# Performance work log

Measured on AMD Instinct MI355X. Metric: run time of the kernel, lower is better.

## Reference

```python
import jax, jax.numpy as jnp
import numpy as np

B, N = 256, 400
DIMENSIONS, VOCAB = 400, 2
T_DIM, H_DIM = 128, 256
EDGE_P = 0.05
LOG_MAX_POS = np.float32(np.log(10000.0))


def timestep_embedding(t, dim):
    # transformer sinusoidal embedding (DDPM/score-SDE style)
    half = dim // 2
    freqs = jnp.exp(-LOG_MAX_POS * jnp.arange(half, dtype=jnp.float32) / (half - 1))
    args = t[:, None] * freqs[None, :]  # [B, half]
    return jnp.concatenate([jnp.sin(args), jnp.cos(args)], axis=-1)  # [B, dim]


def gcn_norm_adj(adj):
    # PyG GCNConv: binary edges (dense_to_sparse values discarded), add self loops,
    # symmetric normalization. deg computed per target (column sums).
    A = (adj != 0).astype(adj.dtype)
    eye = jnp.eye(adj.shape[-1], dtype=adj.dtype)
    As = A + eye[None]                     # [B,N,N]
    deg = As.sum(axis=-2)                  # column sums, [B,N]; >=1 due to self loops
    dis = 1.0 / jnp.sqrt(deg)              # [B,N]
    # out[i] = dis[i] * sum_j As[j,i] * dis[j] * x[j]  ->  An = dis_i * As^T * dis_j
    return dis[:, :, None] * jnp.swapaxes(As, -1, -2) * dis[:, None, :]


def setup_inputs() -> dict:
    key = jax.random.key(0)
    k = jax.random.split(key, 8)
    # symmetric Bernoulli adjacency, no self loops
    up = jnp.triu(jax.random.bernoulli(k[0], EDGE_P, (B, N, N)), 1)
    adj = (up + jnp.swapaxes(up, -1, -2)).astype(jnp.float32)
    times = jax.random.uniform(k[1], (B,), dtype=jnp.float32)
    s = 0.05
    W1 = jax.random.normal(k[2], (T_DIM + 1, H_DIM), jnp.float32) * s
    b1 = jnp.zeros((H_DIM,), jnp.float32)
    W2 = jax.random.normal(k[3], (H_DIM, H_DIM), jnp.float32) * s
    b2 = jnp.zeros((H_DIM,), jnp.float32)
    Wlin = jax.random.normal(k[4], (H_DIM, DIMENSIONS * VOCAB), jnp.float32) * s
    blin = jnp.zeros((DIMENSIONS * VOCAB,), jnp.float32)
    return {"adj": adj, "times": times, "W1": W1, "b1": b1,
            "W2": W2, "b2": b2, "Wlin": Wlin, "blin": blin}


def reference(adj, times, W1, b1, W2, b2, Wlin, blin):
    b, n, _ = adj.shape
    node_degree = adj.sum(axis=1)[..., None]                     # [B,N,1]
    temb = timestep_embedding(times, T_DIM)                      # [B,T_DIM]
    temb = jnp.broadcast_to(temb[:, None, :], (b, n, T_DIM))     # [B,N,T_DIM]
    x = jnp.concatenate([node_degree, temb], axis=-1)            # [B,N,T_DIM+1]

    An = gcn_norm_adj(adj)                                       # [B,N,N]
    h = jnp.einsum('bij,bjh->bih', An, x @ W1) + b1              # GCNConv 1
    h = jax.nn.relu(h)
    h = jnp.einsum('bij,bjh->bih', An, h @ W2) + b2              # GCNConv 2
    h = jax.nn.relu(h)
    pooled = h.mean(axis=1)                                      # global mean pool [B,H]
    logits = pooled @ Wlin + blin                                # [B, D*V]
    return logits.reshape(b, DIMENSIONS, VOCAB)
```

## Files before the change

### kernel.cpp

```cpp
#include <hip/hip_runtime.h>
#include <cstdint>
#include <cstddef>

#define BATCH 256
#define NN 400
#define HH 256
#define TDIM 128
#define HALFD 64
#define OUTD 800
#define BITW 16
#define BMW 13
#define Y2S 424

using short8  = __attribute__((ext_vector_type(8))) short;
using short4v = __attribute__((ext_vector_type(4))) short;
using f32x4   = __attribute__((ext_vector_type(4))) float;

__device__ __forceinline__ short f2bf_trunc(float x) {
  union { float f; unsigned int u; } c; c.f = x; return (short)(c.u >> 16);
}
__device__ __forceinline__ short f2bf_rne(float x) {
  union { float f; unsigned int u; } c; c.f = x;
  unsigned int r = c.u + 0x7FFFu + ((c.u >> 16) & 1u);
  return (short)(r >> 16);
}

__global__ __launch_bounds__(256) void k_prep(const float* __restrict__ adj,
    unsigned int* __restrict__ bits, float* __restrict__ dis,
    float* __restrict__ dd) {
  int bg = blockIdx.x;
  int rbase = blockIdx.y * 16;
  int wv = threadIdx.x >> 6, lane = threadIdx.x & 63;
#pragma unroll
  for (int rr = 0; rr < 4; ++rr) {
    int i = rbase + wv * 4 + rr;
    const float* arow = adj + ((size_t)bg * NN + i) * NN;
    unsigned int b8 = 0; int c = 0;
    if (lane < 50) {
      float4 v0 = *(const float4*)(arow + 8 * lane);
      float4 v1 = *(const float4*)(arow + 8 * lane + 4);
      b8 = (v0.x != 0.f ? 1u : 0u) | (v0.y != 0.f ? 2u : 0u) |
           (v0.z != 0.f ? 4u : 0u) | (v0.w != 0.f ? 8u : 0u) |
           (v1.x != 0.f ? 16u : 0u) | (v1.y != 0.f ? 32u : 0u) |
           (v1.z != 0.f ? 64u : 0u) | (v1.w != 0.f ? 128u : 0u);
      c = __popc(b8);
      if ((i >> 3) == lane) b8 |= 1u << (i & 7);
    }
    int cs = c;
#pragma unroll
    for (int s = 32; s; s >>= 1) cs += __shfl_xor(cs, s);
    unsigned int p0 = (unsigned int)__shfl((int)b8, 4 * lane);
    unsigned int p1 = (unsigned int)__shfl((int)b8, 4 * lane + 1);
    unsigned int p2 = (unsigned int)__shfl((int)b8, 4 * lane + 2);
    unsigned int p3 = (unsigned int)__shfl((int)b8, 4 * lane + 3);
    if (lane < BITW)
      bits[((size_t)bg * NN + i) * BITW + lane] =
          (lane < BMW) ? (p0 | (p1 << 8) | (p2 << 16) | (p3 << 24)) : 0u;
    if (lane == 0) {
      float d = rsqrtf((float)cs + 1.f);
      dis[bg * NN + i] = d;
      dd[bg * NN + i] = d * (float)cs;
    }
  }
}

__global__ __launch_bounds__(256) void k_temb(
    const float* __restrict__ times, const float* __restrict__ W1,
    float* __restrict__ tproj) {
  int b = blockIdx.x, t = threadIdx.x;
  __shared__ float te[TDIM];
  if (t < HALFD) {
    float f = expf(-9.210340371976184f * (float)t / (float)(HALFD - 1));
    float arg = times[b] * f;
    te[t] = sinf(arg);
    te[t + HALFD] = cosf(arg);
  }
  __syncthreads();
  float acc = 0.f;
#pragma unroll 8
  for (int k = 0; k < TDIM; ++k) acc += te[k] * W1[(1 + k) * HH + t];
  tproj[b * HH + t] = acc;
}

__global__ __launch_bounds__(256) void k_w2s(const float* __restrict__ W2,
                                             short* __restrict__ W2s) {
  int t = threadIdx.x;
  int blk = blockIdx.x * 4 + (t >> 6);
  int lane = t & 63;
  int q = blk >> 5, k0 = (blk >> 2) & 7, f = blk & 3;
  int n = q * 64 + f * 16 + (lane & 15);
  int kb = k0 * 32 + (lane >> 4) * 8;
  short8 v;
#pragma unroll
  for (int e = 0; e < 8; ++e) v[e] = f2bf_rne(W2[(size_t)(kb + e) * HH + n]);
  *(short8*)(W2s + (size_t)blk * 512 + lane * 8) = v;
}

__global__ __launch_bounds__(512) void k_pq(const unsigned int* __restrict__ bits,
    const float* __restrict__ dis, const float* __restrict__ dd,
    float* __restrict__ pp, float* __restrict__ qq) {
  int bg = blockIdx.x, t = threadIdx.x;
  __shared__ float sd[NN], su[NN];
  for (int j = t; j < NN; j += 512) { sd[j] = dis[bg * NN + j]; su[j] = dd[bg * NN + j]; }
  __syncthreads();
  if (t >= NN) return;
  const uint4* bp = (const uint4*)(bits + ((size_t)bg * NN + t) * BITW);
  uint4 qa = bp[0], qb = bp[1], qc = bp[2];
  unsigned int wr[13] = {qa.x, qa.y, qa.z, qa.w, qb.x, qb.y, qb.z, qb.w,
                         qc.x, qc.y, qc.z, qc.w, ((const unsigned int*)bp)[12]};
  float ps = 0.f, qs = 0.f;
#pragma unroll
  for (int w = 0; w < BMW; ++w) {
    unsigned int u = wr[w];
    int base = w * 32;
    while (u) {
      int j = base + __builtin_ctz(u);
      u &= u - 1;
      ps += su[j]; qs += sd[j];
    }
  }
  float d = sd[t];
  pp[bg * NN + t] = d * ps;
  qq[bg * NN + t] = d * qs;
}

__global__ __launch_bounds__(512, 2) void k_fused(
    const unsigned int* __restrict__ bits, const float* __restrict__ disg,
    const float* __restrict__ ppg, const float* __restrict__ qqg,
    const short* __restrict__ W2s, const float* __restrict__ W1,
    const float* __restrict__ b1, const float* __restrict__ tproj,
    const float* __restrict__ b2, float* __restrict__ pooled) {
  extern __shared__ char smem[];
  short* y2q         = (short*)smem;
  unsigned int* bmpL = (unsigned int*)(smem + 54272);
  float* sd          = (float*)(smem + 75072);
  float* ppL         = (float*)(smem + 76672);
  float* qqL         = (float*)(smem + 78272);
  short* lut4        = (short*)(smem + 79872);
  float* pool        = (float*)(smem + 76672);

  int t = threadIdx.x;
  int wv = t >> 6, lane = t & 63, l15 = lane & 15, l4 = lane >> 4;
  int bg = blockIdx.x, q = blockIdx.y;

  if (t < NN) {
    const uint4* bp = (const uint4*)(bits + ((size_t)bg * NN + t) * BITW);
    uint4 qa = bp[0], qb = bp[1], qc = bp[2];
    bmpL[t * BMW + 0] = qa.x;  bmpL[t * BMW + 1] = qa.y;
    bmpL[t * BMW + 2] = qa.z;  bmpL[t * BMW + 3] = qa.w;
    bmpL[t * BMW + 4] = qb.x;  bmpL[t * BMW + 5] = qb.y;
    bmpL[t * BMW + 6] = qb.z;  bmpL[t * BMW + 7] = qb.w;
    bmpL[t * BMW + 8] = qc.x;  bmpL[t * BMW + 9] = qc.y;
    bmpL[t * BMW + 10] = qc.z; bmpL[t * BMW + 11] = qc.w;
    bmpL[t * BMW + 12] = ((const unsigned int*)bp)[12];
    sd[t] = disg[bg * NN + t];
    ppL[t] = ppg[bg * NN + t];
    qqL[t] = qqg[bg * NN + t];
  }
  if (t < 192) {
    int n = t / 3, c = t % 3;
    short8 z = {};
    *(short8*)(y2q + n * Y2S + 400 + c * 8) = z;
  }
  if (t < 16) {
    short4v v;
#pragma unroll
    for (int e = 0; e < 4; ++e) v[e] = ((t >> e) & 1) ? (short)0x3F80 : (short)0;
    *(short4v*)(lut4 + t * 4) = v;
  }
  __syncthreads();

  const float* tpr = tproj + bg * HH;
  const short* w2b = W2s + (size_t)q * 8 * 4 * 512;
  float pv[4], qv[4];
#pragma unroll
  for (int mi = 0; mi < 4; ++mi) {
    int mt = wv + mi * 8;
    int arow = mt * 16 + l15;
    pv[mi] = (mt < 25) ? ppL[arow] : 0.f;
    qv[mi] = (mt < 25) ? qqL[arow] : 0.f;
  }
  f32x4 acc[4][4];
#pragma unroll
  for (int mi = 0; mi < 4; ++mi)
#pragma unroll
    for (int f = 0; f < 4; ++f) acc[mi][f] = (f32x4){0.f, 0.f, 0.f, 0.f};

#pragma unroll
  for (int k0 = 0; k0 < 8; ++k0) {
    int kk = k0 * 32 + l4 * 8;
    float4 w1a = *(const float4*)(W1 + kk), w1b = *(const float4*)(W1 + kk + 4);
    float4 b1a = *(const float4*)(b1 + kk), b1b = *(const float4*)(b1 + kk + 4);
    float4 tpa = *(const float4*)(tpr + kk), tpb = *(const float4*)(tpr + kk + 4);
    short8 bf[4];
#pragma unroll
    for (int f = 0; f < 4; ++f)
      bf[f] = *(const short8*)(w2b + (size_t)(k0 * 4 + f) * 512 + lane * 8);
#pragma unroll
    for (int mi = 0; mi < 4; ++mi) {
      if (wv + mi * 8 < 25) {
        float ppv = pv[mi], qqv = qv[mi];
        short8 af;
        af[0] = f2bf_trunc(fmaxf(ppv * w1a.x + qqv * tpa.x + b1a.x, 0.f));
        af[1] = f2bf_trunc(fmaxf(ppv * w1a.y + qqv * tpa.y + b1a.y, 0.f));
        af[2] = f2bf_trunc(fmaxf(ppv * w1a.z + qqv * tpa.z + b1a.z, 0.f));
        af[3] = f2bf_trunc(fmaxf(ppv * w1a.w + qqv * tpa.w + b1a.w, 0.f));
        af[4] = f2bf_trunc(fmaxf(ppv * w1b.x + qqv * tpb.x + b1b.x, 0.f));
        af[5] = f2bf_trunc(fmaxf(ppv * w1b.y + qqv * tpb.y + b1b.y, 0.f));
        af[6] = f2bf_trunc(fmaxf(ppv * w1b.z + qqv * tpb.z + b1b.z, 0.f));
        af[7] = f2bf_trunc(fmaxf(ppv * w1b.w + qqv * tpb.w + b1b.w, 0.f));
#pragma unroll
        for (int f = 0; f < 4; ++f)
          acc[mi][f] = __builtin_amdgcn_mfma_f32_16x16x32_bf16(af, bf[f], acc[mi][f], 0, 0, 0);
      }
    }
  }
#pragma unroll
  for (int mi = 0; mi < 4; ++mi) {
    int mt = wv + mi * 8;
    if (mt < 25) {
      float4 d4 = *(const float4*)(sd + mt * 16 + l4 * 4);
#pragma unroll
      for (int f = 0; f < 4; ++f) {
        short4v pk;
        pk[0] = f2bf_trunc(d4.x * acc[mi][f][0]);
        pk[1] = f2bf_trunc(d4.y * acc[mi][f][1]);
        pk[2] = f2bf_trunc(d4.z * acc[mi][f][2]);
        pk[3] = f2bf_trunc(d4.w * acc[mi][f][3]);
        *(short4v*)(y2q + (f * 16 + l15) * Y2S + mt * 16 + l4 * 4) = pk;
      }
    }
  }
  __syncthreads();

  f32x4 acc2[4][4];
#pragma unroll
  for (int mi = 0; mi < 4; ++mi)
#pragma unroll
    for (int f = 0; f < 4; ++f) acc2[mi][f] = (f32x4){0.f, 0.f, 0.f, 0.f};

#pragma unroll
  for (int ks = 0; ks < 13; ++ks) {
    short8 bfv[4];
#pragma unroll
    for (int f = 0; f < 4; ++f)
      bfv[f] = *(const short8*)(y2q + (f * 16 + l15) * Y2S + ks * 32 + l4 * 8);
#pragma unroll
    for (int mi = 0; mi < 4; ++mi) {
      int mt = wv + mi * 8;
      if (mt < 25) {
        unsigned int wd = bmpL[(mt * 16 + l15) * BMW + ks];
        unsigned int byt = (wd >> (l4 * 8)) & 0xFFu;
        short4v lo = *(const short4v*)(lut4 + (byt & 15u) * 4);
        short4v hi = *(const short4v*)(lut4 + (byt >> 4) * 4);
        short8 af;
        af[0] = lo[0]; af[1] = lo[1]; af[2] = lo[2]; af[3] = lo[3];
        af[4] = hi[0]; af[5] = hi[1]; af[6] = hi[2]; af[7] = hi[3];
#pragma unroll
        for (int f = 0; f < 4; ++f)
          acc2[mi][f] = __builtin_amdgcn_mfma_f32_16x16x32_bf16(af, bfv[f], acc2[mi][f], 0, 0, 0);
      }
    }
  }

#pragma unroll
  for (int f = 0; f < 4; ++f) {
    float b2v = b2[q * 64 + f * 16 + l15];
    float s = 0.f;
#pragma unroll
    for (int mi = 0; mi < 4; ++mi) {
      int mt = wv + mi * 8;
      if (mt < 25) {
        float4 d4 = *(const float4*)(sd + mt * 16 + l4 * 4);
        s += fmaxf(d4.x * acc2[mi][f][0] + b2v, 0.f)
           + fmaxf(d4.y * acc2[mi][f][1] + b2v, 0.f)
           + fmaxf(d4.z * acc2[mi][f][2] + b2v, 0.f)
           + fmaxf(d4.w * acc2[mi][f][3] + b2v, 0.f);
      }
    }
    s += __shfl_xor(s, 16);
    s += __shfl_xor(s, 32);
    if (l4 == 0) pool[wv * 64 + f * 16 + l15] = s;
  }
  __syncthreads();
  if (t < 64) {
    float sum = 0.f;
#pragma unroll
    for (int w8 = 0; w8 < 8; ++w8) sum += pool[w8 * 64 + t];
    pooled[(size_t)bg * HH + q * 64 + t] = sum;
  }
}

__global__ __launch_bounds__(256) void k_out(
    const float* __restrict__ pooled, const float* __restrict__ Wlin,
    const float* __restrict__ blin, float* __restrict__ out) {
  int bb = blockIdx.x * 2, t = threadIdx.x;
  __shared__ float ps[2][HH];
  ps[0][t] = pooled[(size_t)bb * HH + t] * (1.f / 400.f);
  ps[1][t] = pooled[(size_t)(bb + 1) * HH + t] * (1.f / 400.f);
  __syncthreads();
#pragma unroll
  for (int c = 0; c < 4; ++c) {
    int o = t + c * 256;
    if (o < OUTD) {
      float a0 = blin[o], a1 = a0;
#pragma unroll 8
      for (int h = 0; h < HH; ++h) {
        float wv = Wlin[h * OUTD + o];
        a0 += ps[0][h] * wv;
        a1 += ps[1][h] * wv;
      }
      out[(size_t)bb * OUTD + o] = a0;
      out[(size_t)(bb + 1) * OUTD + o] = a1;
    }
  }
}

extern "C" void kernel_launch(void* const* d_in, const int* in_sizes, int n_in,
                              void* d_out, int out_size, void* d_ws, size_t ws_size,
                              hipStream_t stream) {
  const float* adj   = (const float*)d_in[0];
  const float* times = (const float*)d_in[1];
  const float* W1    = (const float*)d_in[2];
  const float* b1    = (const float*)d_in[3];
  const float* W2    = (const float*)d_in[4];
  const float* b2    = (const float*)d_in[5];
  const float* Wlin  = (const float*)d_in[6];
  const float* blin  = (const float*)d_in[7];
  float* out = (float*)d_out;

  char* ws = (char*)d_ws;
  size_t off = 0;
  auto alloc = [&](size_t bytes) -> void* {
    void* ptr = ws + off;
    off = (off + bytes + 255) & ~(size_t)255;
    return ptr;
  };
  float* dis    = (float*)alloc((size_t)BATCH * NN * 4);
  float* dd     = (float*)alloc((size_t)BATCH * NN * 4);
  float* pp     = (float*)alloc((size_t)BATCH * NN * 4);
  float* qq     = (float*)alloc((size_t)BATCH * NN * 4);
  float* tproj  = (float*)alloc((size_t)BATCH * HH * 4);
  float* pooled = (float*)alloc((size_t)BATCH * HH * 4);
  short* W2s    = (short*)alloc((size_t)128 * 512 * 2);
  unsigned int* bits = (unsigned int*)alloc((size_t)BATCH * NN * BITW * 4);

  k_temb<<<BATCH, 256, 0, stream>>>(times, W1, tproj);
  k_w2s<<<32, 256, 0, stream>>>(W2, W2s);
  k_prep<<<dim3(BATCH, 25), 256, 0, stream>>>(adj, bits, dis, dd);
  k_pq<<<BATCH, 512, 0, stream>>>(bits, dis, dd, pp, qq);
  k_fused<<<dim3(BATCH, 4), 512, 80000, stream>>>(
      bits, dis, pp, qq, W2s, W1, b1, tproj, b2, pooled);
  k_out<<<128, 256, 0, stream>>>(pooled, Wlin, blin, out);
}
```

Before: 150.3 us.

## Fold degree and pq computation into fused kernel, merge temb and W2 prep

Removes the separate k_pq kernel and the dis/dd/pp/qq global buffers. The fused kernel now computes degrees from the popcount of the bitmap rows (self loop included) and does the neighbour sums for p/q in shared memory. k_temb and k_w2s are merged into one launch, leaving four launches instead of six. In exchange, each of the 4 column-split blocks per graph redoes the pq computation, and shared memory grows to 81600 bytes.

```diff
diff --git a/kernel.cpp b/kernel.cpp
--- a/kernel.cpp
+++ b/kernel.cpp
@@ -26,8 +26,7 @@
 }
 
 __global__ __launch_bounds__(256) void k_prep(const float* __restrict__ adj,
-    unsigned int* __restrict__ bits, float* __restrict__ dis,
-    float* __restrict__ dd) {
+    unsigned int* __restrict__ bits) {
   int bg = blockIdx.x;
   int rbase = blockIdx.y * 16;
   int wv = threadIdx.x >> 6, lane = threadIdx.x & 63;
@@ -35,7 +34,7 @@
   for (int rr = 0; rr < 4; ++rr) {
     int i = rbase + wv * 4 + rr;
     const float* arow = adj + ((size_t)bg * NN + i) * NN;
-    unsigned int b8 = 0; int c = 0;
+    unsigned int b8 = 0;
     if (lane < 50) {
       float4 v0 = *(const float4*)(arow + 8 * lane);
       float4 v1 = *(const float4*)(arow + 8 * lane + 4);
@@ -43,100 +42,63 @@
            (v0.z != 0.f ? 4u : 0u) | (v0.w != 0.f ? 8u : 0u) |
            (v1.x != 0.f ? 16u : 0u) | (v1.y != 0.f ? 32u : 0u) |
            (v1.z != 0.f ? 64u : 0u) | (v1.w != 0.f ? 128u : 0u);
-      c = __popc(b8);
       if ((i >> 3) == lane) b8 |= 1u << (i & 7);
     }
-    int cs = c;
-#pragma unroll
-    for (int s = 32; s; s >>= 1) cs += __shfl_xor(cs, s);
     unsigned int p0 = (unsigned int)__shfl((int)b8, 4 * lane);
     unsigned int p1 = (unsigned int)__shfl((int)b8, 4 * lane + 1);
     unsigned int p2 = (unsigned int)__shfl((int)b8, 4 * lane + 2);
     unsigned int p3 = (unsigned int)__shfl((int)b8, 4 * lane + 3);
-    if (lane < BITW)
+    if (lane < BMW)
       bits[((size_t)bg * NN + i) * BITW + lane] =
-          (lane < BMW) ? (p0 | (p1 << 8) | (p2 << 16) | (p3 << 24)) : 0u;
-    if (lane == 0) {
-      float d = rsqrtf((float)cs + 1.f);
-      dis[bg * NN + i] = d;
-      dd[bg * NN + i] = d * (float)cs;
-    }
-  }
-}
-
-__global__ __launch_bounds__(256) void k_temb(
+          p0 | (p1 << 8) | (p2 << 16) | (p3 << 24);
+  }
+}
+
+__global__ __launch_bounds__(256) void k_tw(
     const float* __restrict__ times, const float* __restrict__ W1,
-    float* __restrict__ tproj) {
-  int b = blockIdx.x, t = threadIdx.x;
+    float* __restrict__ tproj, const float* __restrict__ W2,
+    short* __restrict__ W2s) {
   __shared__ float te[TDIM];
-  if (t < HALFD) {
-    float f = expf(-9.210340371976184f * (float)t / (float)(HALFD - 1));
-    float arg = times[b] * f;
-    te[t] = sinf(arg);
-    te[t + HALFD] = cosf(arg);
-  }
-  __syncthreads();
-  float acc = 0.f;
+  int t = threadIdx.x;
+  if (blockIdx.x < 256) {
+    int b = blockIdx.x;
+    if (t < HALFD) {
+      float f = expf(-9.210340371976184f * (float)t / (float)(HALFD - 1));
+      float arg = times[b] * f;
+      te[t] = sinf(arg);
+      te[t + HALFD] = cosf(arg);
+    }
+    __syncthreads();
+    float acc = 0.f;
 #pragma unroll 8
-  for (int k = 0; k < TDIM; ++k) acc += te[k] * W1[(1 + k) * HH + t];
-  tproj[b * HH + t] = acc;
-}
-
-__global__ __launch_bounds__(256) void k_w2s(const float* __restrict__ W2,
-                                             short* __restrict__ W2s) {
-  int t = threadIdx.x;
-  int blk = blockIdx.x * 4 + (t >> 6);
-  int lane = t & 63;
-  int q = blk >> 5, k0 = (blk >> 2) & 7, f = blk & 3;
-  int n = q * 64 + f * 16 + (lane & 15);
-  int kb = k0 * 32 + (lane >> 4) * 8;
-  short8 v;
-#pragma unroll
-  for (int e = 0; e < 8; ++e) v[e] = f2bf_rne(W2[(size_t)(kb + e) * HH + n]);
-  *(short8*)(W2s + (size_t)blk * 512 + lane * 8) = v;
-}
-
-__global__ __launch_bounds__(512) void k_pq(const unsigned int* __restrict__ bits,
-    const float* __restrict__ dis, const float* __restrict__ dd,
-    float* __restrict__ pp, float* __restrict__ qq) {
-  int bg = blockIdx.x, t = threadIdx.x;
-  __shared__ float sd[NN], su[NN];
-  for (int j = t; j < NN; j += 512) { sd[j] = dis[bg * NN + j]; su[j] = dd[bg * NN + j]; }
-  __syncthreads();
-  if (t >= NN) return;
-  const uint4* bp = (const uint4*)(bits + ((size_t)bg * NN + t) * BITW);
-  uint4 qa = bp[0], qb = bp[1], qc = bp[2];
-  unsigned int wr[13] = {qa.x, qa.y, qa.z, qa.w, qb.x, qb.y, qb.z, qb.w,
-                         qc.x, qc.y, qc.z, qc.w, ((const unsigned int*)bp)[12]};
-  float ps = 0.f, qs = 0.f;
-#pragma unroll
-  for (int w = 0; w < BMW; ++w) {
-    unsigned int u = wr[w];
-    int base = w * 32;
-    while (u) {
-      int j = base + __builtin_ctz(u);
-      u &= u - 1;
-      ps += su[j]; qs += sd[j];
-    }
-  }
-  float d = sd[t];
-  pp[bg * NN + t] = d * ps;
-  qq[bg * NN + t] = d * qs;
+    for (int k = 0; k < TDIM; ++k) acc += te[k] * W1[(1 + k) * HH + t];
+    tproj[b * HH + t] = acc;
+  } else {
+    int blk = (blockIdx.x - 256) * 4 + (t >> 6);
+    int lane = t & 63;
+    int q = blk >> 5, k0 = (blk >> 2) & 7, f = blk & 3;
+    int n = q * 64 + f * 16 + (lane & 15);
+    int kb = k0 * 32 + (lane >> 4) * 8;
+    short8 v;
+#pragma unroll
+    for (int e = 0; e < 8; ++e) v[e] = f2bf_rne(W2[(size_t)(kb + e) * HH + n]);
+    *(short8*)(W2s + (size_t)blk * 512 + lane * 8) = v;
+  }
 }
 
 __global__ __launch_bounds__(512, 2) void k_fused(
-    const unsigned int* __restrict__ bits, const float* __restrict__ disg,
-    const float* __restrict__ ppg, const float* __restrict__ qqg,
-    const short* __restrict__ W2s, const float* __restrict__ W1,
-    const float* __restrict__ b1, const float* __restrict__ tproj,
-    const float* __restrict__ b2, float* __restrict__ pooled) {
+    const unsigned int* __restrict__ bits, const short* __restrict__ W2s,
+    const float* __restrict__ W1, const float* __restrict__ b1,
+    const float* __restrict__ tproj, const float* __restrict__ b2,
+    float* __restrict__ pooled) {
   extern __shared__ char smem[];
   short* y2q         = (short*)smem;
   unsigned int* bmpL = (unsigned int*)(smem + 54272);
   float* sd          = (float*)(smem + 75072);
-  float* ppL         = (float*)(smem + 76672);
-  float* qqL         = (float*)(smem + 78272);
-  short* lut4        = (short*)(smem + 79872);
+  float* su          = (float*)(smem + 76672);
+  float* ppL         = (float*)(smem + 78272);
+  float* qqL         = (float*)(smem + 79872);
+  short* lut4        = (short*)(smem + 81472);
   float* pool        = (float*)(smem + 76672);
 
   int t = threadIdx.x;
@@ -146,16 +108,21 @@
   if (t < NN) {
     const uint4* bp = (const uint4*)(bits + ((size_t)bg * NN + t) * BITW);
     uint4 qa = bp[0], qb = bp[1], qc = bp[2];
+    unsigned int w12 = ((const unsigned int*)bp)[12];
     bmpL[t * BMW + 0] = qa.x;  bmpL[t * BMW + 1] = qa.y;
     bmpL[t * BMW + 2] = qa.z;  bmpL[t * BMW + 3] = qa.w;
     bmpL[t * BMW + 4] = qb.x;  bmpL[t * BMW + 5] = qb.y;
     bmpL[t * BMW + 6] = qb.z;  bmpL[t * BMW + 7] = qb.w;
     bmpL[t * BMW + 8] = qc.x;  bmpL[t * BMW + 9] = qc.y;
     bmpL[t * BMW + 10] = qc.z; bmpL[t * BMW + 11] = qc.w;
-    bmpL[t * BMW + 12] = ((const unsigned int*)bp)[12];
-    sd[t] = disg[bg * NN + t];
-    ppL[t] = ppg[bg * NN + t];
-    qqL[t] = qqg[bg * NN + t];
+    bmpL[t * BMW + 12] = w12;
+    int pc = __popc(qa.x) + __popc(qa.y) + __popc(qa.z) + __popc(qa.w) +
+             __popc(qb.x) + __popc(qb.y) + __popc(qb.z) + __popc(qb.w) +
+             __popc(qc.x) + __popc(qc.y) + __popc(qc.z) + __popc(qc.w) +
+             __popc(w12);
+    float d = rsqrtf((float)pc);
+    sd[t] = d;
+    su[t] = d * (float)(pc - 1);
   }
   if (t < 192) {
     int n = t / 3, c = t % 3;
@@ -167,6 +134,24 @@
 #pragma unroll
     for (int e = 0; e < 4; ++e) v[e] = ((t >> e) & 1) ? (short)0x3F80 : (short)0;
     *(short4v*)(lut4 + t * 4) = v;
+  }
+  __syncthreads();
+
+  if (t < NN) {
+    float ps = 0.f, qs = 0.f;
+#pragma unroll
+    for (int wi = 0; wi < BMW; ++wi) {
+      unsigned int u = bmpL[t * BMW + wi];
+      int base = wi * 32;
+      while (u) {
+        int j = base + __builtin_ctz(u);
+        u &= u - 1;
+        ps += su[j]; qs += sd[j];
+      }
+    }
+    float d = sd[t];
+    ppL[t] = d * ps;
+    qqL[t] = d * qs;
   }
   __syncthreads();
 
@@ -336,20 +321,14 @@
     off = (off + bytes + 255) & ~(size_t)255;
     return ptr;
   };
-  float* dis    = (float*)alloc((size_t)BATCH * NN * 4);
-  float* dd     = (float*)alloc((size_t)BATCH * NN * 4);
-  float* pp     = (float*)alloc((size_t)BATCH * NN * 4);
-  float* qq     = (float*)alloc((size_t)BATCH * NN * 4);
   float* tproj  = (float*)alloc((size_t)BATCH * HH * 4);
   float* pooled = (float*)alloc((size_t)BATCH * HH * 4);
   short* W2s    = (short*)alloc((size_t)128 * 512 * 2);
   unsigned int* bits = (unsigned int*)alloc((size_t)BATCH * NN * BITW * 4);
 
-  k_temb<<<BATCH, 256, 0, stream>>>(times, W1, tproj);
-  k_w2s<<<32, 256, 0, stream>>>(W2, W2s);
-  k_prep<<<dim3(BATCH, 25), 256, 0, stream>>>(adj, bits, dis, dd);
-  k_pq<<<BATCH, 512, 0, stream>>>(bits, dis, dd, pp, qq);
-  k_fused<<<dim3(BATCH, 4), 512, 80000, stream>>>(
-      bits, dis, pp, qq, W2s, W1, b1, tproj, b2, pooled);
+  k_tw<<<288, 256, 0, stream>>>(times, W1, tproj, W2, W2s);
+  k_prep<<<dim3(BATCH, 25), 256, 0, stream>>>(adj, bits);
+  k_fused<<<dim3(BATCH, 4), 512, 81600, stream>>>(
+      bits, W2s, W1, b1, tproj, b2, pooled);
   k_out<<<128, 256, 0, stream>>>(pooled, Wlin, blin, out);
 }
```

Measured after the change: 158.7 us. +5.6%, slower.
